# Performance work log

Measured on AMD Instinct MI355X. Metric: run time of the kernel, lower is better.

The kernel has to match this reference:

```python
import jax, jax.numpy as jnp
import numpy as np

V, E, H = 32000, 512, 1024
B, T = 32, 64

def setup_inputs() -> dict:
    key = jax.random.key(0)
    ks = jax.random.split(key, 8)
    return {
        "x": jax.random.randint(ks[0], (B, T), 0, V, dtype=jnp.int32),
        "state_h": jax.random.normal(ks[1], (B, H), dtype=jnp.float32),
        "state_c": jax.random.normal(ks[2], (B, H), dtype=jnp.float32),
        "emb_table": jax.random.normal(ks[3], (V, E), dtype=jnp.float32) * 0.02,
        "W": jax.random.normal(ks[4], (E, 4 * H), dtype=jnp.float32) * (1.0 / np.sqrt(E)),
        "U": jax.random.normal(ks[5], (H, 4 * H), dtype=jnp.float32) * (1.0 / np.sqrt(H)),
        "b": jnp.zeros((4 * H,), dtype=jnp.float32),
        "dense_W": jax.random.normal(ks[6], (H, V), dtype=jnp.float32) * (1.0 / np.sqrt(H)),
        "dense_b": jnp.zeros((V,), dtype=jnp.float32),
    }

def _lstm(emb, h0, c0, W, U, b):
    # Precompute input projections for all timesteps: [B,T,4H]
    xW = jnp.einsum('bte,eg->btg', emb, W) + b
    def step(carry, xw_t):
        h, c = carry
        z = xw_t + h @ U  # [B,4H]
        i, f, g, o = jnp.split(z, 4, axis=-1)  # Keras gate order i,f,c,o
        i = jax.nn.sigmoid(i)
        f = jax.nn.sigmoid(f)
        g = jnp.tanh(g)
        o = jax.nn.sigmoid(o)
        c = f * c + i * g
        h = o * jnp.tanh(c)
        return (h, c), h
    (h, c), hs = jax.lax.scan(step, (h0, c0), xW.transpose(1, 0, 2))
    return hs.transpose(1, 0, 2), h, c  # [B,T,H], [B,H], [B,H]

def reference(x, state_h, state_c, emb_table, W, U, b, dense_W, dense_b):
    emb = emb_table[x]  # [B,T,E]
    seq, h, c = _lstm(emb, state_h, state_c, W, U, b)
    logits = jnp.einsum('bth,hv->btv', seq, dense_W) + dense_b  # [B,T,V]
    return logits, h, c
```

## Files before the change

kernel.cpp:

```cpp
#include <hip/hip_runtime.h>

typedef unsigned short u16;
typedef __bf16 bf16x8 __attribute__((ext_vector_type(8)));
typedef float f32x4 __attribute__((ext_vector_type(4)));
typedef u16 u16x8 __attribute__((ext_vector_type(8)));
typedef u16 u16x4 __attribute__((ext_vector_type(4)));

#define T_STEPS 64
#define BATCH 32
#define HDIM 1024
#define EDIM 512
#define VDIM 32000
#define GDIM 4096

__device__ __forceinline__ u16 f2b(float v) {
  unsigned x = __float_as_uint(v);
  return (u16)((x + 0x7fffu + ((x >> 16) & 1u)) >> 16);
}

__device__ __forceinline__ void gload16(const void* g, void* l) {
  __builtin_amdgcn_global_load_lds(
      (const __attribute__((address_space(1))) void*)g,
      (__attribute__((address_space(3))) void*)l, 16, 0, 0);
}

__device__ __forceinline__ f32x4 mfma16(bf16x8 a, bf16x8 b, f32x4 c) {
  return __builtin_amdgcn_mfma_f32_16x16x32_bf16(a, b, c, 0, 0, 0);
}


__global__ __launch_bounds__(256) void gather_emb_k(
    const int* __restrict__ x, const float* __restrict__ emb,
    u16* __restrict__ A) {
  int bt = blockIdx.x;
  int tok = x[bt];
  const float4* src = (const float4*)(emb + (size_t)tok * EDIM);
  u16x4* dst = (u16x4*)(A + (size_t)bt * EDIM);
  if (threadIdx.x < 128) {
    float4 v = src[threadIdx.x];
    u16x4 o = {f2b(v.x), f2b(v.y), f2b(v.z), f2b(v.w)};
    dst[threadIdx.x] = o;
  }
}

__global__ __launch_bounds__(256) void transpose_cvt_k(
    const float* __restrict__ in, u16* __restrict__ out, int K, int N) {
  __shared__ u16 tile[64][80];
  int n0 = blockIdx.x * 64, k0 = blockIdx.y * 64;
  int tid = threadIdx.x;
  int r0 = tid >> 4;
  int c4 = (tid & 15) * 4;
#pragma unroll
  for (int rr = 0; rr < 4; ++rr) {
    int r = rr * 16 + r0;
    float4 v = *reinterpret_cast<const float4*>(
        &in[(size_t)(k0 + r) * N + n0 + c4]);
    tile[c4 + 0][r] = f2b(v.x);
    tile[c4 + 1][r] = f2b(v.y);
    tile[c4 + 2][r] = f2b(v.z);
    tile[c4 + 3][r] = f2b(v.w);
  }
  __syncthreads();
  int wr2 = tid >> 3, c8 = (tid & 7) * 8;
#pragma unroll
  for (int rr = 0; rr < 2; ++rr) {
    int r = rr * 32 + wr2;
    *reinterpret_cast<u16x8*>(&out[(size_t)(n0 + r) * K + k0 + c8]) =
        *reinterpret_cast<const u16x8*>(&tile[r][c8]);
  }
}

__global__ __launch_bounds__(256) void transpose_cvt_permU_k(
    const float* __restrict__ in, u16* __restrict__ out) {
  const int K = HDIM, N = GDIM;
  __shared__ u16 tile[64][80];
  int n0 = blockIdx.x * 64, k0 = blockIdx.y * 64;
  int tid = threadIdx.x;
  int r0 = tid >> 4;
  int c4 = (tid & 15) * 4;
#pragma unroll
  for (int rr = 0; rr < 4; ++rr) {
    int r = rr * 16 + r0;
    float4 v = *reinterpret_cast<const float4*>(
        &in[(size_t)(k0 + r) * N + n0 + c4]);
    tile[c4 + 0][r] = f2b(v.x);
    tile[c4 + 1][r] = f2b(v.y);
    tile[c4 + 2][r] = f2b(v.z);
    tile[c4 + 3][r] = f2b(v.w);
  }
  __syncthreads();
  int wr2 = tid >> 3, c8 = (tid & 7) * 8;
#pragma unroll
  for (int rr = 0; rr < 2; ++rr) {
    int r = rr * 32 + wr2;
    int n = n0 + r;
    int g = n >> 10, c = n & 1023;
    int pn = ((c >> 2) << 4) + (g << 2) + (c & 3);
    *reinterpret_cast<u16x8*>(&out[(size_t)pn * K + k0 + c8]) =
        *reinterpret_cast<const u16x8*>(&tile[r][c8]);
  }
}

__global__ __launch_bounds__(256) void init_state_k(
    const float* __restrict__ h0, const float* __restrict__ c0,
    u16* __restrict__ h0b, float* __restrict__ c_ws) {
  int i = blockIdx.x * 256 + threadIdx.x;
  h0b[i] = f2b(h0[i]);
  c_ws[i] = c0[i];
}


__global__ __launch_bounds__(256) void gemm_bf16_k(
    const u16* __restrict__ A, const u16* __restrict__ BT,
    const float* __restrict__ bias, float* __restrict__ C,
    int M, int N, int K) {
  __shared__ u16 As[128 * 64];
  __shared__ u16 Bs[128 * 64];
  const int tid = threadIdx.x;
  const int w = tid >> 6, lane = tid & 63;
  const int lo16 = lane & 15, hi4 = lane >> 4;
  const int nmb = gridDim.y;
  const int bid = blockIdx.y * gridDim.x + blockIdx.x;
  const int m0 = (bid % nmb) * 128, n0 = (bid / nmb) * 128;
  const int wr = w >> 1, wc = w & 1;
  f32x4 acc[4][4] = {};

  const int srow = lane >> 3;
  const int scol = (lane & 7) * 8;

  for (int k0 = 0; k0 < K; k0 += 64) {
    __syncthreads();
#pragma unroll
    for (int r = 0; r < 4; ++r) {
      int blkrow = (r * 4 + w) * 8 + srow;
      gload16(A + (size_t)(m0 + blkrow) * K + k0 + scol,
              As + (r * 4 + w) * 512);
      gload16(BT + (size_t)(n0 + blkrow) * K + k0 + scol,
              Bs + (r * 4 + w) * 512);
    }
    __syncthreads();

    bf16x8 af[4][2], bfr[4][2];
#pragma unroll
    for (int mi = 0; mi < 4; ++mi)
#pragma unroll
      for (int kk = 0; kk < 2; ++kk)
        af[mi][kk] = *reinterpret_cast<const bf16x8*>(
            As + (wr * 64 + mi * 16 + lo16) * 64 + kk * 32 + hi4 * 8);
#pragma unroll
    for (int nj = 0; nj < 4; ++nj)
#pragma unroll
      for (int kk = 0; kk < 2; ++kk)
        bfr[nj][kk] = *reinterpret_cast<const bf16x8*>(
            Bs + (wc * 64 + nj * 16 + lo16) * 64 + kk * 32 + hi4 * 8);
#pragma unroll
    for (int mi = 0; mi < 4; ++mi)
#pragma unroll
      for (int nj = 0; nj < 4; ++nj)
#pragma unroll
        for (int kk = 0; kk < 2; ++kk)
          acc[mi][nj] = mfma16(af[mi][kk], bfr[nj][kk], acc[mi][nj]);
  }

  const int row0 = m0 + wr * 64, col0 = n0 + wc * 64;
#pragma unroll
  for (int mi = 0; mi < 4; ++mi) {
#pragma unroll
    for (int nj = 0; nj < 4; ++nj) {
      int col = col0 + nj * 16 + lo16;
      float bv = bias ? bias[col] : 0.f;
#pragma unroll
      for (int j = 0; j < 4; ++j) {
        int row = row0 + mi * 16 + hi4 * 4 + j;
        C[(size_t)row * N + col] = acc[mi][nj][j] + bv;
      }
    }
  }
}


#define STG_A(dst, h, kb)                                              \
  do {                                                                 \
    gload16(Abytes + offA[h][0] + (kb), (dst) + (h) * 16384 + w * 1024); \
    gload16(Abytes + offA[h][1] + (kb),                                \
            (dst) + (h) * 16384 + 8192 + w * 1024);                    \
  } while (0)
#define STG_B(dst, h, kb)                                              \
  do {                                                                 \
    gload16(Bbytes + offB[h][0] + (kb),                                \
            (dst) + 32768 + (h) * 16384 + w * 1024);                   \
    gload16(Bbytes + offB[h][1] + (kb),                                \
            (dst) + 32768 + (h) * 16384 + 8192 + w * 1024);            \
  } while (0)
#define VMW4 asm volatile("s_waitcnt vmcnt(4)" ::: "memory")
#define VMW0 asm volatile("s_waitcnt vmcnt(0)" ::: "memory")

#define PHASE(cur, mih, njh, STG, WAIT)                                   \
  do {                                                                    \
    STG;                                                                  \
    bf16x8 af[4][2], bfr[2][2];                                           \
    _Pragma("unroll") for (int u = 0; u < 4; ++u) {                       \
      af[u][0] = *reinterpret_cast<const bf16x8*>((cur) +                 \
                                                  aoff[(mih)*4 + u][0]);  \
      af[u][1] = *reinterpret_cast<const bf16x8*>((cur) +                 \
                                                  aoff[(mih)*4 + u][1]);  \
    }                                                                     \
    _Pragma("unroll") for (int v = 0; v < 2; ++v) {                       \
      bfr[v][0] = *reinterpret_cast<const bf16x8*>((cur) +                \
                                                   boff[(njh)*2 + v][0]); \
      bfr[v][1] = *reinterpret_cast<const bf16x8*>((cur) +                \
                                                   boff[(njh)*2 + v][1]); \
    }                                                                     \
    __builtin_amdgcn_s_barrier();                                         \
    asm volatile("s_waitcnt lgkmcnt(0)" ::: "memory");                    \
    __builtin_amdgcn_s_setprio(1);                                        \
    _Pragma("unroll") for (int u = 0; u < 4; ++u)                         \
        _Pragma("unroll") for (int v = 0; v < 2; ++v) {                   \
      acc[(mih)*4 + u][(njh)*2 + v] =                                     \
          mfma16(af[u][0], bfr[v][0], acc[(mih)*4 + u][(njh)*2 + v]);     \
      acc[(mih)*4 + u][(njh)*2 + v] =                                     \
          mfma16(af[u][1], bfr[v][1], acc[(mih)*4 + u][(njh)*2 + v]);     \
    }                                                                     \
    __builtin_amdgcn_s_setprio(0);                                        \
    WAIT;                                                                 \
    __builtin_amdgcn_s_barrier();                                         \
  } while (0)

__global__ __launch_bounds__(512, 2) void gemm256_k(
    const u16* __restrict__ A,
    const u16* __restrict__ BT,
    const float* __restrict__ bias,
    float* __restrict__ C,
    int M, int N, int K) {
  __shared__ __attribute__((aligned(1024))) char smem[131072];
  const int tid = threadIdx.x;
  const int w = tid >> 6, lane = tid & 63;
  const int lo16 = lane & 15, hi4 = lane >> 4;
  const int wr = w >> 2, wc = w & 3;

  const int cpx = gridDim.x >> 3;
  const int bid = blockIdx.x;
  const int swz = (bid & 7) * cpx + (bid >> 3);
  const int nmb = M >> 8;
  const int m0 = (swz % nmb) << 8, n0 = (swz / nmb) << 8;

  const char* Abytes = (const char*)A;
  const char* Bbytes = (const char*)BT;
  const int K2 = K * 2;

  int offA[2][2], offB[2][2];
#pragma unroll
  for (int h = 0; h < 2; ++h)
#pragma unroll
    for (int i = 0; i < 2; ++i) {
      int o = h * 16384 + (i * 512 + tid) * 16;
      int s = o >> 10, q = o & 1023;
      int qp = q ^ (((q >> 9) & 1) << 5);
      int row = ((s >> 1) << 4) + (qp >> 6);
      int colb = ((s & 1) << 6) + (qp & 63);
      offA[h][i] = (m0 + row) * K2 + colb;
      offB[h][i] = (n0 + row) * K2 + colb;
    }

  int aoff[8][2], boff[4][2];
#pragma unroll
  for (int mi = 0; mi < 8; ++mi)
#pragma unroll
    for (int kk = 0; kk < 2; ++kk) {
      int r = (mi >> 2) * 128 + wr * 64 + (mi & 3) * 16 + lo16;
      int q = (r & 15) * 64 + hi4 * 16;
      int qs = q ^ (((q >> 9) & 1) << 5);
      aoff[mi][kk] = (((r >> 4) << 1) + kk) * 1024 + qs;
    }
#pragma unroll
  for (int nj = 0; nj < 4; ++nj)
#pragma unroll
    for (int kk = 0; kk < 2; ++kk) {
      int r = (nj >> 1) * 128 + wc * 32 + (nj & 1) * 16 + lo16;
      int q = (r & 15) * 64 + hi4 * 16;
      int qs = q ^ (((q >> 9) & 1) << 5);
      boff[nj][kk] = 32768 + (((r >> 4) << 1) + kk) * 1024 + qs;
    }

  f32x4 acc[8][4] = {};
  char* const bd = smem;
  char* const bo = smem + 65536;

  STG_A(bd, 0, 0);
  STG_B(bd, 0, 0);
  STG_A(bd, 1, 0);
  STG_B(bd, 1, 0);
  STG_A(bo, 0, 128);
  STG_B(bo, 0, 128);
  VMW4;
  __builtin_amdgcn_s_barrier();

  const int NITER = K >> 7;
  for (int it = 0; it < NITER - 1; ++it) {
    const int k1 = (it * 128 + 64) * 2;
    const int k2 = (it * 128 + 128) * 2;
    const int k3 = (it * 128 + 192) * 2;
    PHASE(bd, 0, 0, STG_A(bo, 1, k1), ((void)0));
    PHASE(bd, 0, 1, STG_B(bo, 1, k1), ((void)0));
    PHASE(bd, 1, 0, STG_A(bd, 0, k2), ((void)0));
    PHASE(bd, 1, 1, STG_B(bd, 0, k2), VMW4);
    PHASE(bo, 0, 0, STG_A(bd, 1, k2), ((void)0));
    PHASE(bo, 0, 1, STG_B(bd, 1, k2), ((void)0));
    PHASE(bo, 1, 0, STG_A(bo, 0, k3), ((void)0));
    PHASE(bo, 1, 1, STG_B(bo, 0, k3), VMW4);
  }
  {
    const int k1 = ((NITER - 1) * 128 + 64) * 2;
    PHASE(bd, 0, 0, STG_A(bo, 1, k1), ((void)0));
    PHASE(bd, 0, 1, STG_B(bo, 1, k1), ((void)0));
    PHASE(bd, 1, 0, ((void)0), ((void)0));
    PHASE(bd, 1, 1, ((void)0), VMW0);
    PHASE(bo, 0, 0, ((void)0), ((void)0));
    PHASE(bo, 0, 1, ((void)0), ((void)0));
    PHASE(bo, 1, 0, ((void)0), ((void)0));
    PHASE(bo, 1, 1, ((void)0), ((void)0));
  }

#pragma unroll
  for (int mi = 0; mi < 8; ++mi) {
    int row = m0 + (mi >> 2) * 128 + wr * 64 + (mi & 3) * 16 + hi4 * 4;
#pragma unroll
    for (int nj = 0; nj < 4; ++nj) {
      int col = n0 + (nj >> 1) * 128 + wc * 32 + (nj & 1) * 16 + lo16;
      float bv = bias ? bias[col] : 0.f;
#pragma unroll
      for (int j = 0; j < 4; ++j)
        C[(size_t)(row + j) * N + col] = acc[mi][nj][j] + bv;
    }
  }
}


__global__ __launch_bounds__(256) void lstm_step2_k(
    const float* __restrict__ xW,
    const u16* __restrict__ h_src,
    const u16* __restrict__ UT2,
    float* __restrict__ c_ws,
    u16* __restrict__ h_dst,
    u16* __restrict__ seq,
    float* __restrict__ out_hc,
    int t) {
  __shared__ float Zs[4][16][17];
  const int tid = threadIdx.x;
  const int w = tid >> 6, lane = tid & 63;
  const int lo16 = lane & 15, hi4 = lane >> 4;
  const int zt = blockIdx.x >> 1;
  const int bt = blockIdx.x & 1;

  const int bb = tid >> 2, jg = tid & 3;
  float xw0 = 0.f, xw1 = 0.f, xw2 = 0.f, xw3 = 0.f;
  if (tid < 64) {
    const float* xrow =
        xW + (size_t)((bt * 16 + bb) * T_STEPS + t) * GDIM + zt * 4 + jg;
    xw0 = xrow[0];
    xw1 = xrow[1024];
    xw2 = xrow[2048];
    xw3 = xrow[3072];
  }

  const u16* arow = h_src + (size_t)(bt * 16 + lo16) * HDIM;
  const u16* brow = UT2 + (size_t)(zt * 16 + lo16) * HDIM;

  f32x4 acc = {};
#pragma unroll
  for (int kc = 0; kc < 8; ++kc) {
    int k = w * 256 + kc * 32 + hi4 * 8;
    bf16x8 a = *reinterpret_cast<const bf16x8*>(arow + k);
    bf16x8 b = *reinterpret_cast<const bf16x8*>(brow + k);
    acc = mfma16(a, b, acc);
  }
#pragma unroll
  for (int j = 0; j < 4; ++j) Zs[w][hi4 * 4 + j][lo16] = acc[j];
  __syncthreads();

  if (tid < 64) {
    int b = bt * 16 + bb;
    int hcol = zt * 4 + jg;
    float z[4] = {xw0, xw1, xw2, xw3};
#pragma unroll
    for (int g = 0; g < 4; ++g)
#pragma unroll
      for (int ww = 0; ww < 4; ++ww) z[g] += Zs[ww][bb][g * 4 + jg];
    size_t cidx = (size_t)b * HDIM + hcol;
    float c_old = c_ws[cidx];
    float ig = 1.f / (1.f + __expf(-z[0]));
    float fg = 1.f / (1.f + __expf(-z[1]));
    float gg = tanhf(z[2]);
    float og = 1.f / (1.f + __expf(-z[3]));
    float cn = fg * c_old + ig * gg;
    float hn = og * tanhf(cn);
    c_ws[cidx] = cn;
    u16 hb = f2b(hn);
    h_dst[cidx] = hb;
    seq[(size_t)(b * T_STEPS + t) * HDIM + hcol] = hb;
    if (out_hc) {
      out_hc[cidx] = hn;
      out_hc[BATCH * HDIM + cidx] = cn;
    }
  }
}


extern "C" void kernel_launch(void* const* d_in, const int* in_sizes, int n_in,
                              void* d_out, int out_size, void* d_ws,
                              size_t ws_size, hipStream_t stream) {
  const int* x = (const int*)d_in[0];
  const float* state_h = (const float*)d_in[1];
  const float* state_c = (const float*)d_in[2];
  const float* emb = (const float*)d_in[3];
  const float* W = (const float*)d_in[4];
  const float* U = (const float*)d_in[5];
  const float* bvec = (const float*)d_in[6];
  const float* dW = (const float*)d_in[7];
  const float* db = (const float*)d_in[8];
  float* out = (float*)d_out;
  char* ws = (char*)d_ws;

  size_t off = 0;
  auto alloc = [&](size_t bytes) {
    void* p = ws + off;
    off += (bytes + 255) & ~(size_t)255;
    return p;
  };
  u16* A_emb = (u16*)alloc(2048ull * EDIM * 2);
  u16* WbT   = (u16*)alloc((size_t)GDIM * EDIM * 2);
  u16* UT2   = (u16*)alloc((size_t)GDIM * HDIM * 2);
  u16* DbT   = (u16*)alloc((size_t)VDIM * HDIM * 2);
  float* xW  = (float*)alloc(2048ull * GDIM * 4);
  u16* seq   = (u16*)alloc(2048ull * HDIM * 2);
  u16* h0b   = (u16*)alloc((size_t)BATCH * HDIM * 2);
  u16* hbuf  = (u16*)alloc(2ull * BATCH * HDIM * 2);
  float* c_ws = (float*)alloc((size_t)BATCH * HDIM * 4);
  if (off > ws_size) return;

  gather_emb_k<<<2048, 256, 0, stream>>>(x, emb, A_emb);
  transpose_cvt_k<<<dim3(GDIM / 64, EDIM / 64), 256, 0, stream>>>(W, WbT, EDIM, GDIM);
  transpose_cvt_permU_k<<<dim3(GDIM / 64, HDIM / 64), 256, 0, stream>>>(U, UT2);
  transpose_cvt_k<<<dim3(VDIM / 64, HDIM / 64), 256, 0, stream>>>(dW, DbT, HDIM, VDIM);
  init_state_k<<<128, 256, 0, stream>>>(state_h, state_c, h0b, c_ws);

  gemm_bf16_k<<<dim3(GDIM / 128, 2048 / 128), 256, 0, stream>>>(
      A_emb, WbT, bvec, xW, 2048, GDIM, EDIM);

  for (int t = 0; t < T_STEPS; ++t) {
    const u16* h_src = (t == 0) ? h0b : (hbuf + (size_t)(t & 1) * (BATCH * HDIM));
    u16* h_dst = hbuf + (size_t)((t + 1) & 1) * (BATCH * HDIM);
    float* outhc = (t == T_STEPS - 1) ? (out + 65536000ull) : nullptr;
    lstm_step2_k<<<512, 256, 0, stream>>>(xW, h_src, UT2, c_ws, h_dst, seq,
                                          outhc, t);
  }

  gemm256_k<<<dim3((2048 / 256) * (VDIM / 256)), 512, 0, stream>>>(
      seq, DbT, db, out, 2048, VDIM, HDIM);
}
```

Before: 667.1 us.

## Merge GEMM phases to reuse B fragments and read LSTM h from seq

Measured after the change: 653.2 us. 1.02x faster.

```diff
diff --git a/kernel.cpp b/kernel.cpp
--- a/kernel.cpp
+++ b/kernel.cpp
@@ -195,33 +195,51 @@
 #define VMW4 asm volatile("s_waitcnt vmcnt(4)" ::: "memory")
 #define VMW0 asm volatile("s_waitcnt vmcnt(0)" ::: "memory")
 
-#define PHASE(cur, mih, njh, STG, WAIT)                                   \
+#define MFMA_BLOCK(mih)                                                   \
   do {                                                                    \
-    STG;                                                                  \
-    bf16x8 af[4][2], bfr[2][2];                                           \
+    __builtin_amdgcn_s_setprio(1);                                        \
+    _Pragma("unroll") for (int u = 0; u < 4; ++u)                         \
+        _Pragma("unroll") for (int v = 0; v < 4; ++v) {                   \
+      acc[(mih)*4 + u][v] = mfma16(af[u][0], bfr[v][0], acc[(mih)*4 + u][v]); \
+      acc[(mih)*4 + u][v] = mfma16(af[u][1], bfr[v][1], acc[(mih)*4 + u][v]); \
+    }                                                                     \
+    __builtin_amdgcn_s_setprio(0);                                        \
+  } while (0)
+
+#define PH_FULL(cur, mih, STG, WAIT)                                      \
+  do {                                                                    \
+    bf16x8 af[4][2];                                                      \
     _Pragma("unroll") for (int u = 0; u < 4; ++u) {                       \
       af[u][0] = *reinterpret_cast<const bf16x8*>((cur) +                 \
                                                   aoff[(mih)*4 + u][0]);  \
       af[u][1] = *reinterpret_cast<const bf16x8*>((cur) +                 \
                                                   aoff[(mih)*4 + u][1]);  \
     }                                                                     \
-    _Pragma("unroll") for (int v = 0; v < 2; ++v) {                       \
-      bfr[v][0] = *reinterpret_cast<const bf16x8*>((cur) +                \
-                                                   boff[(njh)*2 + v][0]); \
-      bfr[v][1] = *reinterpret_cast<const bf16x8*>((cur) +                \
-                                                   boff[(njh)*2 + v][1]); \
+    _Pragma("unroll") for (int v = 0; v < 4; ++v) {                       \
+      bfr[v][0] = *reinterpret_cast<const bf16x8*>((cur) + boff[v][0]);   \
+      bfr[v][1] = *reinterpret_cast<const bf16x8*>((cur) + boff[v][1]);   \
     }                                                                     \
+    STG;                                                                  \
     __builtin_amdgcn_s_barrier();                                         \
     asm volatile("s_waitcnt lgkmcnt(0)" ::: "memory");                    \
-    __builtin_amdgcn_s_setprio(1);                                        \
-    _Pragma("unroll") for (int u = 0; u < 4; ++u)                         \
-        _Pragma("unroll") for (int v = 0; v < 2; ++v) {                   \
-      acc[(mih)*4 + u][(njh)*2 + v] =                                     \
-          mfma16(af[u][0], bfr[v][0], acc[(mih)*4 + u][(njh)*2 + v]);     \
-      acc[(mih)*4 + u][(njh)*2 + v] =                                     \
-          mfma16(af[u][1], bfr[v][1], acc[(mih)*4 + u][(njh)*2 + v]);     \
+    MFMA_BLOCK(mih);                                                      \
+    WAIT;                                                                 \
+    __builtin_amdgcn_s_barrier();                                         \
+  } while (0)
+
+#define PH_A(cur, mih, STG, WAIT)                                         \
+  do {                                                                    \
+    bf16x8 af[4][2];                                                      \
+    _Pragma("unroll") for (int u = 0; u < 4; ++u) {                       \
+      af[u][0] = *reinterpret_cast<const bf16x8*>((cur) +                 \
+                                                  aoff[(mih)*4 + u][0]);  \
+      af[u][1] = *reinterpret_cast<const bf16x8*>((cur) +                 \
+                                                  aoff[(mih)*4 + u][1]);  \
     }                                                                     \
-    __builtin_amdgcn_s_setprio(0);                                        \
+    STG;                                                                  \
+    __builtin_amdgcn_s_barrier();                                         \
+    asm volatile("s_waitcnt lgkmcnt(0)" ::: "memory");                    \
+    MFMA_BLOCK(mih);                                                      \
     WAIT;                                                                 \
     __builtin_amdgcn_s_barrier();                                         \
   } while (0)
@@ -283,6 +301,7 @@
     }
 
   f32x4 acc[8][4] = {};
+  bf16x8 bfr[4][2];
   char* const bd = smem;
   char* const bo = smem + 65536;
 
@@ -300,25 +319,17 @@
     const int k1 = (it * 128 + 64) * 2;
     const int k2 = (it * 128 + 128) * 2;
     const int k3 = (it * 128 + 192) * 2;
-    PHASE(bd, 0, 0, STG_A(bo, 1, k1), ((void)0));
-    PHASE(bd, 0, 1, STG_B(bo, 1, k1), ((void)0));
-    PHASE(bd, 1, 0, STG_A(bd, 0, k2), ((void)0));
-    PHASE(bd, 1, 1, STG_B(bd, 0, k2), VMW4);
-    PHASE(bo, 0, 0, STG_A(bd, 1, k2), ((void)0));
-    PHASE(bo, 0, 1, STG_B(bd, 1, k2), ((void)0));
-    PHASE(bo, 1, 0, STG_A(bo, 0, k3), ((void)0));
-    PHASE(bo, 1, 1, STG_B(bo, 0, k3), VMW4);
+    PH_FULL(bd, 0, { STG_A(bo, 1, k1); STG_B(bo, 1, k1); }, ((void)0));
+    PH_A(bd, 1, { STG_A(bd, 0, k2); STG_B(bd, 0, k2); }, VMW4);
+    PH_FULL(bo, 0, { STG_A(bd, 1, k2); STG_B(bd, 1, k2); }, ((void)0));
+    PH_A(bo, 1, { STG_A(bo, 0, k3); STG_B(bo, 0, k3); }, VMW4);
   }
   {
     const int k1 = ((NITER - 1) * 128 + 64) * 2;
-    PHASE(bd, 0, 0, STG_A(bo, 1, k1), ((void)0));
-    PHASE(bd, 0, 1, STG_B(bo, 1, k1), ((void)0));
-    PHASE(bd, 1, 0, ((void)0), ((void)0));
-    PHASE(bd, 1, 1, ((void)0), VMW0);
-    PHASE(bo, 0, 0, ((void)0), ((void)0));
-    PHASE(bo, 0, 1, ((void)0), ((void)0));
-    PHASE(bo, 1, 0, ((void)0), ((void)0));
-    PHASE(bo, 1, 1, ((void)0), ((void)0));
+    PH_FULL(bd, 0, { STG_A(bo, 1, k1); STG_B(bo, 1, k1); }, ((void)0));
+    PH_A(bd, 1, ((void)0), VMW0);
+    PH_FULL(bo, 0, ((void)0), ((void)0));
+    PH_A(bo, 1, ((void)0), ((void)0));
   }
 
 #pragma unroll
@@ -339,9 +350,9 @@
 __global__ __launch_bounds__(256) void lstm_step2_k(
     const float* __restrict__ xW,
     const u16* __restrict__ h_src,
+    int h_stride,
     const u16* __restrict__ UT2,
     float* __restrict__ c_ws,
-    u16* __restrict__ h_dst,
     u16* __restrict__ seq,
     float* __restrict__ out_hc,
     int t) {
@@ -363,7 +374,7 @@
     xw3 = xrow[3072];
   }
 
-  const u16* arow = h_src + (size_t)(bt * 16 + lo16) * HDIM;
+  const u16* arow = h_src + (size_t)(bt * 16 + lo16) * h_stride;
   const u16* brow = UT2 + (size_t)(zt * 16 + lo16) * HDIM;
 
   f32x4 acc = {};
@@ -395,9 +406,7 @@
     float cn = fg * c_old + ig * gg;
     float hn = og * tanhf(cn);
     c_ws[cidx] = cn;
-    u16 hb = f2b(hn);
-    h_dst[cidx] = hb;
-    seq[(size_t)(b * T_STEPS + t) * HDIM + hcol] = hb;
+    seq[(size_t)(b * T_STEPS + t) * HDIM + hcol] = f2b(hn);
     if (out_hc) {
       out_hc[cidx] = hn;
       out_hc[BATCH * HDIM + cidx] = cn;
@@ -434,7 +443,6 @@
   float* xW  = (float*)alloc(2048ull * GDIM * 4);
   u16* seq   = (u16*)alloc(2048ull * HDIM * 2);
   u16* h0b   = (u16*)alloc((size_t)BATCH * HDIM * 2);
-  u16* hbuf  = (u16*)alloc(2ull * BATCH * HDIM * 2);
   float* c_ws = (float*)alloc((size_t)BATCH * HDIM * 4);
   if (off > ws_size) return;
 
@@ -448,10 +456,10 @@
       A_emb, WbT, bvec, xW, 2048, GDIM, EDIM);
 
   for (int t = 0; t < T_STEPS; ++t) {
-    const u16* h_src = (t == 0) ? h0b : (hbuf + (size_t)(t & 1) * (BATCH * HDIM));
-    u16* h_dst = hbuf + (size_t)((t + 1) & 1) * (BATCH * HDIM);
+    const u16* h_src = (t == 0) ? h0b : (seq + (size_t)(t - 1) * HDIM);
+    int h_stride = (t == 0) ? HDIM : T_STEPS * HDIM;
     float* outhc = (t == T_STEPS - 1) ? (out + 65536000ull) : nullptr;
-    lstm_step2_k<<<512, 256, 0, stream>>>(xW, h_src, UT2, c_ws, h_dst, seq,
+    lstm_step2_k<<<512, 256, 0, stream>>>(xW, h_src, h_stride, UT2, c_ws, seq,
                                           outhc, t);
   }
 
```
